# Kernel optimization log

Hardware: AMD Instinct MI355X
Metric: run time of the kernel (lower is better)

The kernel has to match this reference:

```python
import jax, jax.numpy as jnp
import numpy as np

CH = 512
NUM_HEADS = 8
NUM_GROUPS = 32  # min(32, channels)
EPS = 1e-5


def setup_inputs() -> dict:
    key = jax.random.key(0)
    ks = jax.random.split(key, 4)
    B, C, H, W = 8, CH, 32, 32
    x = jax.random.normal(ks[0], (B, C, H, W), dtype=jnp.float32)
    gn_weight = jnp.ones((C,), dtype=jnp.float32)
    gn_bias = jnp.zeros((C,), dtype=jnp.float32)
    # 1x1 conv weights stored as [out_ch, in_ch] (kernel dims squeezed)
    qkv_weight = jax.random.normal(ks[1], (3 * C, C), dtype=jnp.float32) * (C ** -0.5)
    qkv_bias = jnp.zeros((3 * C,), dtype=jnp.float32)
    proj_weight = jax.random.normal(ks[2], (C, C), dtype=jnp.float32) * (C ** -0.5)
    proj_bias = jnp.zeros((C,), dtype=jnp.float32)
    return {
        "x": x,
        "gn_weight": gn_weight,
        "gn_bias": gn_bias,
        "qkv_weight": qkv_weight,
        "qkv_bias": qkv_bias,
        "proj_weight": proj_weight,
        "proj_bias": proj_bias,
    }


def _group_norm(x, weight, bias):
    B, C, H, W = x.shape
    g = x.reshape(B, NUM_GROUPS, C // NUM_GROUPS, H, W)
    mean = jnp.mean(g, axis=(2, 3, 4), keepdims=True)
    var = jnp.var(g, axis=(2, 3, 4), keepdims=True)
    g = (g - mean) * jax.lax.rsqrt(var + EPS)
    g = g.reshape(B, C, H, W)
    return g * weight[None, :, None, None] + bias[None, :, None, None]


def reference(x, gn_weight, gn_bias, qkv_weight, qkv_bias, proj_weight, proj_bias):
    B, C, H, W = x.shape
    nh = NUM_HEADS
    hc = C // nh
    N = H * W

    h = _group_norm(x, gn_weight, gn_bias)
    # 1x1 conv == per-pixel matmul
    qkv = jnp.einsum('oc,bchw->bohw', qkv_weight, h) + qkv_bias[None, :, None, None]
    q, k, v = jnp.split(qkv, 3, axis=1)
    # b (h c) x y -> b h c (x y)
    q = q.reshape(B, nh, hc, N)
    k = k.reshape(B, nh, hc, N)
    v = v.reshape(B, nh, hc, N)

    scale = hc ** -0.5
    attn = jnp.einsum('bhci,bhcj->bhij', q, k) * scale  # [B, nh, N, N]
    attn = jax.nn.softmax(attn, axis=-1)
    out = jnp.einsum('bhij,bhcj->bhci', attn, v)  # [B, nh, hc, N]
    out = out.reshape(B, C, H, W)
    out = jnp.einsum('oc,bchw->bohw', proj_weight, out) + proj_bias[None, :, None, None]
    return x + out
```

## Files before the change

### kernel.cpp

```cpp
#include <hip/hip_runtime.h>
#include <math.h>

#define B_   8
#define C_   512
#define N_   1024
#define NH_  8
#define HC_  64

typedef __attribute__((ext_vector_type(8))) short bf16x8;
typedef __attribute__((ext_vector_type(4))) float f32x4;
typedef __attribute__((ext_vector_type(16))) float f32x16;

#define MFMA16(a, b, c) __builtin_amdgcn_mfma_f32_16x16x32_bf16(a, b, c, 0, 0, 0)
#define MFMA32(a, b, c) __builtin_amdgcn_mfma_f32_32x32x16_bf16(a, b, c, 0, 0, 0)

__device__ __forceinline__ unsigned short f2bf(float f) {
  unsigned u = __builtin_bit_cast(unsigned, f);
  u += 0x7fffu + ((u >> 16) & 1u);
  return (unsigned short)(u >> 16);
}

__device__ __forceinline__ unsigned pack2(float a, float b) {
  return (unsigned)f2bf(a) | ((unsigned)f2bf(b) << 16);
}

__device__ __forceinline__ void gll16(const void* g, void* l) {
  __builtin_amdgcn_global_load_lds(
      (const __attribute__((address_space(1))) unsigned int*)g,
      (__attribute__((address_space(3))) unsigned int*)l, 16, 0, 0);
}

__global__ __launch_bounds__(256) void prep(const float* __restrict__ x,
                                            const float* __restrict__ gw,
                                            const float* __restrict__ gb,
                                            const float* __restrict__ qkvw,
                                            const float* __restrict__ pw,
                                            unsigned short* __restrict__ hT,
                                            unsigned short* __restrict__ qkvw_bf,
                                            unsigned short* __restrict__ projw_bf) {
  const int t = threadIdx.x;
  if (blockIdx.x >= 256) {
    const int widx = blockIdx.x - 256;
    const float* src = (widx < 768) ? qkvw : pw;
    unsigned short* dst = (widx < 768) ? qkvw_bf : projw_bf;
    const int i = ((widx < 768) ? widx : widx - 768) * 1024 + t * 4;
    const float4 v = *(const float4*)(src + i);
    ushort4 o;
    o.x = f2bf(v.x); o.y = f2bf(v.y); o.z = f2bf(v.z); o.w = f2bf(v.w);
    *(ushort4*)(dst + i) = o;
    return;
  }
  const int b = blockIdx.x >> 5;
  const int g = blockIdx.x & 31;
  const float* xg = x + ((size_t)b * C_ + (size_t)g * 16) * N_;

  float4 xv[16];
  float s = 0.f, ss = 0.f;
#pragma unroll
  for (int k = 0; k < 16; ++k) {
    xv[k] = *(const float4*)(xg + (size_t)k * N_ + t * 4);
    s  += xv[k].x + xv[k].y + xv[k].z + xv[k].w;
    ss += xv[k].x * xv[k].x + xv[k].y * xv[k].y + xv[k].z * xv[k].z + xv[k].w * xv[k].w;
  }
#pragma unroll
  for (int off = 32; off > 0; off >>= 1) {
    s  += __shfl_down(s, off);
    ss += __shfl_down(ss, off);
  }
  __shared__ float rs[4], rss[4], sh_mi[2];
  if ((t & 63) == 0) { rs[t >> 6] = s; rss[t >> 6] = ss; }
  __syncthreads();
  if (t == 0) {
    s  = rs[0] + rs[1] + rs[2] + rs[3];
    ss = rss[0] + rss[1] + rss[2] + rss[3];
    const float mean = s * (1.f / 16384.f);
    const float var  = ss * (1.f / 16384.f) - mean * mean;
    sh_mi[0] = mean;
    sh_mi[1] = rsqrtf(var + 1e-5f);
  }
  __syncthreads();
  const float mean = sh_mi[0], inv = sh_mi[1];

  float sc[16], of[16];
#pragma unroll
  for (int k = 0; k < 16; ++k) {
    const int c = g * 16 + k;
    sc[k] = inv * gw[c];
    of[k] = gb[c] - mean * sc[k];
  }
#pragma unroll
  for (int r = 0; r < 4; ++r) {
    const int p = t * 4 + r;
    unsigned short* dst = hT + ((size_t)b * N_ + p) * C_ + g * 16;
    uint4 o0, o1;
#pragma unroll
    for (int k2 = 0; k2 < 4; ++k2) {
      const float a0 = ((const float*)&xv[k2 * 2 + 0])[r] * sc[k2 * 2 + 0] + of[k2 * 2 + 0];
      const float a1 = ((const float*)&xv[k2 * 2 + 1])[r] * sc[k2 * 2 + 1] + of[k2 * 2 + 1];
      ((unsigned*)&o0)[k2] = pack2(a0, a1);
      const float b0 = ((const float*)&xv[8 + k2 * 2 + 0])[r] * sc[8 + k2 * 2 + 0] + of[8 + k2 * 2 + 0];
      const float b1 = ((const float*)&xv[8 + k2 * 2 + 1])[r] * sc[8 + k2 * 2 + 1] + of[8 + k2 * 2 + 1];
      ((unsigned*)&o1)[k2] = pack2(b0, b1);
    }
    *(uint4*)(dst)     = o0;
    *(uint4*)(dst + 8) = o1;
  }
}

__global__ __launch_bounds__(256, 3) void gemm_qkv(
    const unsigned short* __restrict__ A, const float* __restrict__ bias,
    const unsigned short* __restrict__ BT, unsigned short* __restrict__ qkTout,
    unsigned short* __restrict__ kfrag, unsigned short* __restrict__ vfrag) {
  __shared__ __attribute__((aligned(16))) short lds[128 * 136];
  const int t = threadIdx.x;
  const int lane = t & 63, w = t >> 6;
  const int lm = lane & 15, q = lane >> 4;
  const int wm = w >> 1, wn = w & 1;
  const int b = blockIdx.z;
  const int m0 = blockIdx.y * 128, n0 = blockIdx.x * 128;
  const unsigned short* Bb = BT + (size_t)b * N_ * C_;

  f32x4 acc[4][4];
#pragma unroll
  for (int i = 0; i < 4; ++i)
#pragma unroll
    for (int j = 0; j < 4; ++j) acc[i][j] = (f32x4){0.f, 0.f, 0.f, 0.f};

#define QKV_STAGE(k0, base_)                                                   \
  {                                                                            \
    _Pragma("unroll") for (int rr = 0; rr < 2; ++rr) {                         \
      const int rg = w * 2 + rr;                                               \
      gll16(A  + (size_t)(m0 + rg * 16 + lm) * C_ + (k0) + q * 8,              \
            (base_) + rg * 512);                                               \
      gll16(Bb + (size_t)(n0 + rg * 16 + lm) * C_ + (k0) + q * 8,              \
            (base_) + (8 + rg) * 512);                                         \
    }                                                                          \
  }

#define QKV_COMPUTE(base_)                                                     \
  {                                                                            \
    bf16x8 af[4];                                                              \
    _Pragma("unroll") for (int mi = 0; mi < 4; ++mi)                           \
      af[mi] = *(const bf16x8*)((base_) + (wm * 4 + mi) * 512 + lane * 8);     \
    _Pragma("unroll") for (int ni = 0; ni < 4; ++ni) {                         \
      const bf16x8 bfr =                                                       \
          *(const bf16x8*)((base_) + (8 + wn * 4 + ni) * 512 + lane * 8);      \
      _Pragma("unroll") for (int mi = 0; mi < 4; ++mi)                         \
        acc[mi][ni] = MFMA16(af[mi], bfr, acc[mi][ni]);                        \
    }                                                                          \
  }

  QKV_STAGE(0, lds)
  for (int it = 0; it < 15; ++it) {
    __syncthreads();
    short* nxt = lds + ((it + 1) & 1) * 8192;
    QKV_STAGE((it + 1) * 32, nxt)
    const short* cur = lds + (it & 1) * 8192;
    QKV_COMPUTE(cur)
  }
  __syncthreads();
  QKV_COMPUTE(lds + 8192)
#undef QKV_STAGE
#undef QKV_COMPUTE

  __syncthreads();
  if (blockIdx.y < 8) {
    const float qs = (blockIdx.y < 4) ? 0.18033688011112042f : 1.0f;
#pragma unroll
    for (int mi = 0; mi < 4; ++mi) {
#pragma unroll
      for (int ni = 0; ni < 4; ++ni) {
        const int pl = wn * 64 + ni * 16 + lm;
        const int ol0 = wm * 64 + mi * 16 + q * 4;
        ushort4 o4;
        o4.x = f2bf((acc[mi][ni][0] + bias[m0 + ol0 + 0]) * qs);
        o4.y = f2bf((acc[mi][ni][1] + bias[m0 + ol0 + 1]) * qs);
        o4.z = f2bf((acc[mi][ni][2] + bias[m0 + ol0 + 2]) * qs);
        o4.w = f2bf((acc[mi][ni][3] + bias[m0 + ol0 + 3]) * qs);
        *(ushort4*)&lds[pl * 136 + ol0] = o4;
      }
    }
    __syncthreads();
    if (blockIdx.y < 4) {
#pragma unroll
      for (int u = 0; u < 8; ++u) {
        const int flat = u * 256 + t;
        const int oc = flat & 15, pl = flat >> 4;
        *(uint4*)&qkTout[((size_t)b * N_ + n0 + pl) * 1024 + m0 + oc * 8] =
            *(const uint4*)&lds[pl * 136 + oc * 8];
      }
    } else {
      const int hh0 = (blockIdx.y - 4) * 2;
#pragma unroll
      for (int u = 0; u < 8; ++u) {
        const int flat = u * 256 + t;
        const int ll = flat & 63, kc = (flat >> 6) & 3;
        const int jbl = (flat >> 8) & 3, hhl = flat >> 10;
        *(uint4*)&kfrag[((((size_t)b * 8 + hh0 + hhl) * 32 + (n0 >> 5) + jbl) * 4 +
                         kc) * 512 + ll * 8] =
            *(const uint4*)&lds[(jbl * 32 + (ll & 31)) * 136 + hhl * 64 +
                                kc * 16 + (ll >> 5) * 8];
      }
    }
  } else {
#pragma unroll
    for (int mi = 0; mi < 4; ++mi)
#pragma unroll
      for (int ni = 0; ni < 4; ++ni) {
        const int pl = wn * 64 + ni * 16 + lm;
#pragma unroll
        for (int r = 0; r < 4; ++r) {
          const int ol = wm * 64 + mi * 16 + q * 4 + r;
          lds[ol * 136 + pl] = f2bf(acc[mi][ni][r] + bias[m0 + ol]);
        }
      }
    __syncthreads();
    const int hh0 = (blockIdx.y - 8) * 2;
#pragma unroll
    for (int u = 0; u < 8; ++u) {
      const int flat = u * 256 + t;
      const int ll = flat & 63, kj = (flat >> 6) & 3;
      const int jtl = (flat >> 8) & 1, nc = (flat >> 9) & 1, hhl = flat >> 10;
      *(uint4*)&vfrag[(((((size_t)b * 8 + hh0 + hhl) * 16 + (n0 >> 6) + jtl) * 2 +
                        nc) * 4 + kj) * 512 + ll * 8] =
          *(const uint4*)&lds[(hhl * 64 + nc * 32 + (ll & 31)) * 136 +
                              jtl * 64 + kj * 16 + (ll >> 5) * 8];
    }
  }
}

__global__ __launch_bounds__(256, 4) void gemm_proj(
    const unsigned short* __restrict__ A, const float* __restrict__ bias,
    const unsigned short* __restrict__ BT, const float* __restrict__ resid,
    float* __restrict__ outf) {
  __shared__ __attribute__((aligned(16))) short lds[32 * 512];
  const int t = threadIdx.x;
  const int lane = t & 63, w = t >> 6;
  const int lm = lane & 15, q = lane >> 4;
  const int wm = w >> 1, wn = w & 1;
  const int b = blockIdx.z;
  const int m0 = blockIdx.y * 64, n0 = blockIdx.x * 64;
  const unsigned short* Bb = BT + (size_t)b * N_ * C_;

  f32x4 acc[2][2];
#pragma unroll
  for (int i = 0; i < 2; ++i)
#pragma unroll
    for (int j = 0; j < 2; ++j) acc[i][j] = (f32x4){0.f, 0.f, 0.f, 0.f};

  for (int k0 = 0; k0 < C_; k0 += 128) {
    __syncthreads();
#pragma unroll
    for (int ks = 0; ks < 4; ++ks) {
      gll16(A  + (size_t)(m0 + w * 16 + lm) * C_ + k0 + ks * 32 + q * 8,
            lds + (w * 4 + ks) * 512);
      gll16(Bb + (size_t)(n0 + w * 16 + lm) * C_ + k0 + ks * 32 + q * 8,
            lds + (16 + w * 4 + ks) * 512);
    }
    __syncthreads();
#pragma unroll
    for (int ks = 0; ks < 4; ++ks) {
      bf16x8 af[2];
#pragma unroll
      for (int mi = 0; mi < 2; ++mi)
        af[mi] = *(const bf16x8*)(lds + ((wm * 2 + mi) * 4 + ks) * 512 + lane * 8);
#pragma unroll
      for (int ni = 0; ni < 2; ++ni) {
        const bf16x8 bfr =
            *(const bf16x8*)(lds + (16 + (wn * 2 + ni) * 4 + ks) * 512 + lane * 8);
#pragma unroll
        for (int mi = 0; mi < 2; ++mi)
          acc[mi][ni] = MFMA16(af[mi], bfr, acc[mi][ni]);
      }
    }
  }

#pragma unroll
  for (int mi = 0; mi < 2; ++mi)
#pragma unroll
    for (int ni = 0; ni < 2; ++ni) {
      const int col = n0 + wn * 32 + ni * 16 + lm;
#pragma unroll
      for (int r = 0; r < 4; ++r) {
        const int row = m0 + wm * 32 + mi * 16 + q * 4 + r;
        const size_t oi = ((size_t)b * 512 + row) * N_ + col;
        outf[oi] = acc[mi][ni][r] + bias[row] + resid[oi];
      }
    }
}

__global__ __launch_bounds__(256, 2) void attn_mfma(
    const unsigned short* __restrict__ qkT, const unsigned short* __restrict__ kfrag,
    const unsigned short* __restrict__ vfrag, unsigned short* __restrict__ aoT) {
  __shared__ __attribute__((aligned(16))) short lds[21504];
  short* Ks = lds;
  short* Vs = lds + 8192;
  short* Pb = lds + 12288;

  const int t = threadIdx.x;
  const int l = t & 63, w = t >> 6;
  const int l31 = l & 31, lh = l >> 5;
  const int id = blockIdx.x;
  const int xcd = id & 7, slot = id >> 3;
  const int pair = xcd * 8 + (slot >> 3);
  const int b = pair >> 3, hh = pair & 7;
  const int i0 = (slot & 7) * 128;

  const unsigned short* QT = qkT + (size_t)b * N_ * 1024;
  const unsigned short* kb = kfrag + (size_t)(b * 8 + hh) * 65536;
  const unsigned short* vb = vfrag + (size_t)(b * 8 + hh) * 65536;
  short* Pw = Pb + w * 2304;

  bf16x8 af[4];
#pragma unroll
  for (int kc = 0; kc < 4; ++kc)
    af[kc] = *(const bf16x8*)(QT + (size_t)(i0 + w * 32 + l31) * 1024 +
                              hh * 64 + kc * 16 + lh * 8);

  f32x16 accO[2];
#pragma unroll
  for (int r2 = 0; r2 < 16; ++r2) { accO[0][r2] = 0.f; accO[1][r2] = 0.f; }
  float lrun = 0.f;

#pragma unroll
  for (int rr = 0; rr < 2; ++rr) {
    const int idx = w * 2 + rr;
    gll16(kb + (size_t)idx * 512 + l * 8, Ks + idx * 512);
  }

  for (int jt = 0; jt < 16; ++jt) {
    __syncthreads();
#pragma unroll
    for (int rr = 0; rr < 2; ++rr) {
      const int idx = w * 2 + rr;
      gll16(vb + ((size_t)jt * 8 + idx) * 512 + l * 8, Vs + idx * 512);
    }
    if (jt < 15) {
#pragma unroll
      for (int rr = 0; rr < 2; ++rr) {
        const int idx = w * 2 + rr;
        gll16(kb + ((size_t)(jt + 1) * 8 + idx) * 512 + l * 8,
              Ks + ((jt + 1) & 1) * 4096 + idx * 512);
      }
    }
    const short* Kc = Ks + (jt & 1) * 4096;

    f32x16 accS[2];
#pragma unroll
    for (int r2 = 0; r2 < 16; ++r2) { accS[0][r2] = 0.f; accS[1][r2] = 0.f; }
    __builtin_amdgcn_s_setprio(1);
#pragma unroll
    for (int kc = 0; kc < 4; ++kc)
#pragma unroll
      for (int jb = 0; jb < 2; ++jb) {
        const bf16x8 kfr = *(const bf16x8*)(Kc + (jb * 4 + kc) * 512 + l * 8);
        accS[jb] = MFMA32(kfr, af[kc], accS[jb]);
      }
    __builtin_amdgcn_s_setprio(0);

    uint4 pa4[4];
#pragma unroll
    for (int jb = 0; jb < 2; ++jb) {
      float p[16];
#pragma unroll
      for (int rg = 0; rg < 16; ++rg) {
        p[rg] = __builtin_exp2f(accS[jb][rg]);
        lrun += p[rg];
      }
      unsigned own[8];
#pragma unroll
      for (int i2 = 0; i2 < 8; ++i2)
        asm("v_cvt_pk_bf16_f32 %0, %1, %2"
            : "=v"(own[i2]) : "v"(p[2 * i2]), "v"(p[2 * i2 + 1]));
#pragma unroll
      for (int m = 0; m < 2; ++m) {
        unsigned x0 = own[4 * m + 0], y0 = own[4 * m + 2];
        unsigned x1 = own[4 * m + 1], y1 = own[4 * m + 3];
        asm("v_permlane32_swap_b32 %0, %1" : "+v"(x0), "+v"(y0));
        asm("v_permlane32_swap_b32 %0, %1" : "+v"(x1), "+v"(y1));
        pa4[jb * 2 + m] = (uint4){x0, x1, y0, y1};
      }
    }

    __syncthreads();

    __builtin_amdgcn_s_setprio(1);
#pragma unroll
    for (int kj = 0; kj < 4; ++kj) {
      const bf16x8 pf = __builtin_bit_cast(bf16x8, pa4[kj]);
#pragma unroll
      for (int nc = 0; nc < 2; ++nc) {
        const bf16x8 vf = *(const bf16x8*)(Vs + (nc * 4 + kj) * 512 + l * 8);
        accO[nc] = MFMA32(pf, vf, accO[nc]);
      }
    }
    __builtin_amdgcn_s_setprio(0);
  }

  const float lr = lrun + __shfl_xor(lrun, 32);
  float* lw = (float*)Pw;
  lw[l31] = 1.f / lr;
  float linvr[16];
#pragma unroll
  for (int rg = 0; rg < 16; ++rg)
    linvr[rg] = lw[(rg & 3) + ((rg >> 2) << 3) + (lh << 2)];

#pragma unroll
  for (int nc = 0; nc < 2; ++nc)
#pragma unroll
    for (int rg = 0; rg < 16; ++rg) {
      const int rowi = (rg & 3) + ((rg >> 2) << 3) + (lh << 2);
      Pw[rowi * 72 + nc * 32 + l31] = (short)f2bf(accO[nc][rg] * linvr[rg]);
    }
  unsigned short* aob = aoT + (size_t)b * N_ * C_;
#pragma unroll
  for (int u = 0; u < 4; ++u) {
    const int flat = u * 64 + l;
    const int c8 = flat & 7, row = flat >> 3;
    *(uint4*)&aob[(size_t)(i0 + w * 32 + row) * C_ + hh * 64 + c8 * 8] =
        *(const uint4*)&Pw[row * 72 + c8 * 8];
  }
}

extern "C" void kernel_launch(void* const* d_in, const int* in_sizes, int n_in,
                              void* d_out, int out_size, void* d_ws, size_t ws_size,
                              hipStream_t stream) {
  const float* x    = (const float*)d_in[0];
  const float* gw   = (const float*)d_in[1];
  const float* gb   = (const float*)d_in[2];
  const float* qkvw = (const float*)d_in[3];
  const float* qkvb = (const float*)d_in[4];
  const float* pw   = (const float*)d_in[5];
  const float* pb   = (const float*)d_in[6];
  float* out = (float*)d_out;

  unsigned short* hT       = (unsigned short*)d_ws;
  unsigned short* qkvw_bf  = hT + (size_t)B_ * N_ * C_;
  unsigned short* projw_bf = qkvw_bf + 1536 * 512;
  unsigned short* qkT      = projw_bf + 512 * 512;
  unsigned short* aoTp     = qkT + (size_t)B_ * N_ * 1024;
  unsigned short* kfrag    = aoTp + (size_t)B_ * N_ * C_;
  unsigned short* vfrag    = kfrag + (size_t)64 * 65536;

  prep<<<1280, 256, 0, stream>>>(x, gw, gb, qkvw, pw, hT, qkvw_bf, projw_bf);
  gemm_qkv<<<dim3(8, 12, B_), 256, 0, stream>>>(qkvw_bf, qkvb, hT, qkT, kfrag, vfrag);
  attn_mfma<<<512, 256, 0, stream>>>(qkT, kfrag, vfrag, aoTp);
  gemm_proj<<<dim3(16, 8, B_), 256, 0, stream>>>(projw_bf, pb, aoTp, x, out);
}
```

Baseline: 161.5 us.

## Double the attention KV tile to 128 columns and raise occupancy hint

Each iteration of the attention kernel now processes 128 key/value columns instead of 64, halving the number of loop iterations and block-wide barriers. K stays double-buffered and V uses a larger single buffer. The output staging area now reuses the K/V shared memory after the loop instead of having its own region. The launch bound requests 3 blocks per CU, which increases LDS use per block and tightens the register budget, so spills are possible.

```diff
diff --git a/kernel.cpp b/kernel.cpp
--- a/kernel.cpp
+++ b/kernel.cpp
@@ -289,13 +289,12 @@
     }
 }
 
-__global__ __launch_bounds__(256, 2) void attn_mfma(
+__global__ __launch_bounds__(256, 3) void attn_mfma(
     const unsigned short* __restrict__ qkT, const unsigned short* __restrict__ kfrag,
     const unsigned short* __restrict__ vfrag, unsigned short* __restrict__ aoT) {
-  __shared__ __attribute__((aligned(16))) short lds[21504];
+  __shared__ __attribute__((aligned(16))) short lds[24576];
   short* Ks = lds;
-  short* Vs = lds + 8192;
-  short* Pb = lds + 12288;
+  short* Vs = lds + 16384;
 
   const int t = threadIdx.x;
   const int l = t & 63, w = t >> 6;
@@ -309,7 +308,6 @@
   const unsigned short* QT = qkT + (size_t)b * N_ * 1024;
   const unsigned short* kb = kfrag + (size_t)(b * 8 + hh) * 65536;
   const unsigned short* vb = vfrag + (size_t)(b * 8 + hh) * 65536;
-  short* Pw = Pb + w * 2304;
 
   bf16x8 af[4];
 #pragma unroll
@@ -323,48 +321,39 @@
   float lrun = 0.f;
 
 #pragma unroll
-  for (int rr = 0; rr < 2; ++rr) {
-    const int idx = w * 2 + rr;
-    gll16(kb + (size_t)idx * 512 + l * 8, Ks + idx * 512);
-  }
-
-  for (int jt = 0; jt < 16; ++jt) {
-    __syncthreads();
-#pragma unroll
-    for (int rr = 0; rr < 2; ++rr) {
-      const int idx = w * 2 + rr;
-      gll16(vb + ((size_t)jt * 8 + idx) * 512 + l * 8, Vs + idx * 512);
-    }
-    if (jt < 15) {
-#pragma unroll
-      for (int rr = 0; rr < 2; ++rr) {
-        const int idx = w * 2 + rr;
-        gll16(kb + ((size_t)(jt + 1) * 8 + idx) * 512 + l * 8,
-              Ks + ((jt + 1) & 1) * 4096 + idx * 512);
-      }
-    }
-    const short* Kc = Ks + (jt & 1) * 4096;
-
-    f32x16 accS[2];
-#pragma unroll
-    for (int r2 = 0; r2 < 16; ++r2) { accS[0][r2] = 0.f; accS[1][r2] = 0.f; }
+  for (int rr = 0; rr < 4; ++rr)
+    gll16(kb + (size_t)(w * 4 + rr) * 512 + l * 8, Ks + (w * 4 + rr) * 512);
+
+  for (int jt = 0; jt < 8; ++jt) {
+    __syncthreads();
+#pragma unroll
+    for (int rr = 0; rr < 4; ++rr)
+      gll16(vb + ((size_t)jt * 16 + w * 4 + rr) * 512 + l * 8,
+            Vs + (w * 4 + rr) * 512);
+    if (jt < 7) {
+#pragma unroll
+      for (int rr = 0; rr < 4; ++rr)
+        gll16(kb + ((size_t)(jt + 1) * 16 + w * 4 + rr) * 512 + l * 8,
+              Ks + ((jt + 1) & 1) * 8192 + (w * 4 + rr) * 512);
+    }
+    const short* Kc = Ks + (jt & 1) * 8192;
+
+    uint4 pa4[8];
     __builtin_amdgcn_s_setprio(1);
 #pragma unroll
-    for (int kc = 0; kc < 4; ++kc)
-#pragma unroll
-      for (int jb = 0; jb < 2; ++jb) {
+    for (int jb = 0; jb < 4; ++jb) {
+      f32x16 accS;
+#pragma unroll
+      for (int r2 = 0; r2 < 16; ++r2) accS[r2] = 0.f;
+#pragma unroll
+      for (int kc = 0; kc < 4; ++kc) {
         const bf16x8 kfr = *(const bf16x8*)(Kc + (jb * 4 + kc) * 512 + l * 8);
-        accS[jb] = MFMA32(kfr, af[kc], accS[jb]);
-      }
-    __builtin_amdgcn_s_setprio(0);
-
-    uint4 pa4[4];
-#pragma unroll
-    for (int jb = 0; jb < 2; ++jb) {
+        accS = MFMA32(kfr, af[kc], accS);
+      }
       float p[16];
 #pragma unroll
       for (int rg = 0; rg < 16; ++rg) {
-        p[rg] = __builtin_exp2f(accS[jb][rg]);
+        p[rg] = __builtin_exp2f(accS[rg]);
         lrun += p[rg];
       }
       unsigned own[8];
@@ -381,22 +370,25 @@
         pa4[jb * 2 + m] = (uint4){x0, x1, y0, y1};
       }
     }
+    __builtin_amdgcn_s_setprio(0);
 
     __syncthreads();
 
     __builtin_amdgcn_s_setprio(1);
 #pragma unroll
-    for (int kj = 0; kj < 4; ++kj) {
-      const bf16x8 pf = __builtin_bit_cast(bf16x8, pa4[kj]);
+    for (int kjg = 0; kjg < 8; ++kjg) {
+      const bf16x8 pf = __builtin_bit_cast(bf16x8, pa4[kjg]);
 #pragma unroll
       for (int nc = 0; nc < 2; ++nc) {
-        const bf16x8 vf = *(const bf16x8*)(Vs + (nc * 4 + kj) * 512 + l * 8);
+        const int g = ((kjg >> 2) << 3) + nc * 4 + (kjg & 3);
+        const bf16x8 vf = *(const bf16x8*)(Vs + g * 512 + l * 8);
         accO[nc] = MFMA32(pf, vf, accO[nc]);
       }
     }
     __builtin_amdgcn_s_setprio(0);
   }
 
+  short* Pw = lds + w * 2304;
   const float lr = lrun + __shfl_xor(lrun, 32);
   float* lw = (float*)Pw;
   lw[l31] = 1.f / lr;
```

After: 161.6 us. Within noise of the previous version (+0.0%).

## Split group-norm into stats and LDS-transposed apply; stage proj epilogue through LDS

Applied to the files above, without the earlier changes.

Group-norm now runs in two kernels. The first computes only per-group mean and inverse std. A new kernel re-reads x, normalizes it, and transposes it through an LDS tile so the bf16 hT writes are coalesced 16-byte rows instead of scattered 32-byte strided stores. The projection GEMM epilogue also stages its accumulators in LDS so the residual read and output write use float4 coalesced accesses. The cost is an extra kernel launch, a second full read of x, and extra LDS traffic and barriers.

```diff
diff --git a/kernel.cpp b/kernel.cpp
--- a/kernel.cpp
+++ b/kernel.cpp
@@ -31,11 +31,9 @@
 }
 
 __global__ __launch_bounds__(256) void prep(const float* __restrict__ x,
-                                            const float* __restrict__ gw,
-                                            const float* __restrict__ gb,
                                             const float* __restrict__ qkvw,
                                             const float* __restrict__ pw,
-                                            unsigned short* __restrict__ hT,
+                                            float2* __restrict__ gstats,
                                             unsigned short* __restrict__ qkvw_bf,
                                             unsigned short* __restrict__ projw_bf) {
   const int t = threadIdx.x;
@@ -54,20 +52,19 @@
   const int g = blockIdx.x & 31;
   const float* xg = x + ((size_t)b * C_ + (size_t)g * 16) * N_;
 
-  float4 xv[16];
   float s = 0.f, ss = 0.f;
 #pragma unroll
   for (int k = 0; k < 16; ++k) {
-    xv[k] = *(const float4*)(xg + (size_t)k * N_ + t * 4);
-    s  += xv[k].x + xv[k].y + xv[k].z + xv[k].w;
-    ss += xv[k].x * xv[k].x + xv[k].y * xv[k].y + xv[k].z * xv[k].z + xv[k].w * xv[k].w;
+    const float4 v = *(const float4*)(xg + (size_t)k * N_ + t * 4);
+    s  += v.x + v.y + v.z + v.w;
+    ss += v.x * v.x + v.y * v.y + v.z * v.z + v.w * v.w;
   }
 #pragma unroll
   for (int off = 32; off > 0; off >>= 1) {
     s  += __shfl_down(s, off);
     ss += __shfl_down(ss, off);
   }
-  __shared__ float rs[4], rss[4], sh_mi[2];
+  __shared__ float rs[4], rss[4];
   if ((t & 63) == 0) { rs[t >> 6] = s; rss[t >> 6] = ss; }
   __syncthreads();
   if (t == 0) {
@@ -75,35 +72,44 @@
     ss = rss[0] + rss[1] + rss[2] + rss[3];
     const float mean = s * (1.f / 16384.f);
     const float var  = ss * (1.f / 16384.f) - mean * mean;
-    sh_mi[0] = mean;
-    sh_mi[1] = rsqrtf(var + 1e-5f);
-  }
-  __syncthreads();
-  const float mean = sh_mi[0], inv = sh_mi[1];
-
-  float sc[16], of[16];
-#pragma unroll
-  for (int k = 0; k < 16; ++k) {
-    const int c = g * 16 + k;
-    sc[k] = inv * gw[c];
-    of[k] = gb[c] - mean * sc[k];
-  }
-#pragma unroll
-  for (int r = 0; r < 4; ++r) {
-    const int p = t * 4 + r;
-    unsigned short* dst = hT + ((size_t)b * N_ + p) * C_ + g * 16;
-    uint4 o0, o1;
-#pragma unroll
-    for (int k2 = 0; k2 < 4; ++k2) {
-      const float a0 = ((const float*)&xv[k2 * 2 + 0])[r] * sc[k2 * 2 + 0] + of[k2 * 2 + 0];
-      const float a1 = ((const float*)&xv[k2 * 2 + 1])[r] * sc[k2 * 2 + 1] + of[k2 * 2 + 1];
-      ((unsigned*)&o0)[k2] = pack2(a0, a1);
-      const float b0 = ((const float*)&xv[8 + k2 * 2 + 0])[r] * sc[8 + k2 * 2 + 0] + of[8 + k2 * 2 + 0];
-      const float b1 = ((const float*)&xv[8 + k2 * 2 + 1])[r] * sc[8 + k2 * 2 + 1] + of[8 + k2 * 2 + 1];
-      ((unsigned*)&o1)[k2] = pack2(b0, b1);
-    }
-    *(uint4*)(dst)     = o0;
-    *(uint4*)(dst + 8) = o1;
+    gstats[b * 32 + g] = make_float2(mean, rsqrtf(var + 1e-5f));
+  }
+}
+
+__global__ __launch_bounds__(256) void prep2(const float* __restrict__ x,
+                                             const float* __restrict__ gw,
+                                             const float* __restrict__ gb,
+                                             const float2* __restrict__ gstats,
+                                             unsigned short* __restrict__ hT) {
+  __shared__ __attribute__((aligned(16))) short tile[32 * 136];
+  const int t = threadIdx.x;
+  const int b = blockIdx.x >> 5;
+  const int px0 = (blockIdx.x & 31) * 32;
+
+  for (int chunk = 0; chunk < 4; ++chunk) {
+    const int ch0 = chunk * 128;
+    if (chunk) __syncthreads();
+#pragma unroll
+    for (int it = 0; it < 4; ++it) {
+      const int c = ch0 + (t >> 3) + it * 32;
+      const int pxl = (t & 7) * 4;
+      const float4 v = *(const float4*)(x + ((size_t)b * C_ + c) * N_ + px0 + pxl);
+      const float2 mi = gstats[b * 32 + (c >> 4)];
+      const float sc = mi.y * gw[c];
+      const float of = gb[c] - mi.x * sc;
+      tile[(pxl + 0) * 136 + (c - ch0)] = (short)f2bf(v.x * sc + of);
+      tile[(pxl + 1) * 136 + (c - ch0)] = (short)f2bf(v.y * sc + of);
+      tile[(pxl + 2) * 136 + (c - ch0)] = (short)f2bf(v.z * sc + of);
+      tile[(pxl + 3) * 136 + (c - ch0)] = (short)f2bf(v.w * sc + of);
+    }
+    __syncthreads();
+#pragma unroll
+    for (int u = 0; u < 2; ++u) {
+      const int flat = u * 256 + t;
+      const int cc8 = flat & 15, pxl = flat >> 4;
+      *(uint4*)&hT[((size_t)b * N_ + px0 + pxl) * C_ + ch0 + cc8 * 8] =
+          *(const uint4*)&tile[pxl * 136 + cc8 * 8];
+    }
   }
 }
 
@@ -275,18 +281,32 @@
     }
   }
 
+  __syncthreads();
+  float* fl = (float*)lds;
 #pragma unroll
   for (int mi = 0; mi < 2; ++mi)
 #pragma unroll
     for (int ni = 0; ni < 2; ++ni) {
-      const int col = n0 + wn * 32 + ni * 16 + lm;
+      const int col_l = wn * 32 + ni * 16 + lm;
 #pragma unroll
       for (int r = 0; r < 4; ++r) {
-        const int row = m0 + wm * 32 + mi * 16 + q * 4 + r;
-        const size_t oi = ((size_t)b * 512 + row) * N_ + col;
-        outf[oi] = acc[mi][ni][r] + bias[row] + resid[oi];
-      }
-    }
+        const int row_l = wm * 32 + mi * 16 + q * 4 + r;
+        fl[row_l * 68 + col_l] = acc[mi][ni][r] + bias[m0 + row_l];
+      }
+    }
+  __syncthreads();
+#pragma unroll
+  for (int u = 0; u < 4; ++u) {
+    const int flat = u * 256 + t;
+    const int c4 = flat & 15, row_l = flat >> 4;
+    const size_t oi = ((size_t)b * 512 + m0 + row_l) * N_ + n0 + c4 * 4;
+    const float4 rv = *(const float4*)(resid + oi);
+    const float4 av = *(const float4*)(fl + row_l * 68 + c4 * 4);
+    float4 ov;
+    ov.x = av.x + rv.x; ov.y = av.y + rv.y;
+    ov.z = av.z + rv.z; ov.w = av.w + rv.w;
+    *(float4*)(outf + oi) = ov;
+  }
 }
 
 __global__ __launch_bounds__(256, 2) void attn_mfma(
@@ -441,8 +461,10 @@
   unsigned short* aoTp     = qkT + (size_t)B_ * N_ * 1024;
   unsigned short* kfrag    = aoTp + (size_t)B_ * N_ * C_;
   unsigned short* vfrag    = kfrag + (size_t)64 * 65536;
-
-  prep<<<1280, 256, 0, stream>>>(x, gw, gb, qkvw, pw, hT, qkvw_bf, projw_bf);
+  float2* gstats           = (float2*)(vfrag + (size_t)64 * 65536);
+
+  prep<<<1280, 256, 0, stream>>>(x, qkvw, pw, gstats, qkvw_bf, projw_bf);
+  prep2<<<256, 256, 0, stream>>>(x, gw, gb, gstats, hT);
   gemm_qkv<<<dim3(8, 12, B_), 256, 0, stream>>>(qkvw_bf, qkvb, hT, qkT, kfrag, vfrag);
   attn_mfma<<<512, 256, 0, stream>>>(qkT, kfrag, vfrag, aoTp);
   gemm_proj<<<dim3(16, 8, B_), 256, 0, stream>>>(projw_bf, pb, aoTp, x, out);
```

Result: no change. 164.3 us (+1.7%).
